# Kernel optimization log

Measured on AMD Instinct MI355X. Metric: run time of the kernel, lower is better.

Reference implementation:

```python
import jax, jax.numpy as jnp
import numpy as np
import math

EMBED = 512
KDIM = 512
VDIM = 512
H = 8
HD = EMBED // H
N = 2048
L = 2048
B = 4


def setup_inputs() -> dict:
    key = jax.random.key(0)
    ks = jax.random.split(key, 14)
    s = 1.0 / math.sqrt(EMBED)
    return {
        "q": jax.random.normal(ks[0], (N, B, EMBED), jnp.float32),
        "k": jax.random.normal(ks[1], (L, B, KDIM), jnp.float32),
        "v": jax.random.normal(ks[2], (L, B, VDIM), jnp.float32),
        "pe1": jax.random.normal(ks[3], (B, N, 3), jnp.float32),
        "pe2": jax.random.normal(ks[4], (L, 3), jnp.float32),
        "Wq": jax.random.normal(ks[5], (EMBED, EMBED), jnp.float32) * s,
        "bq": jnp.zeros((EMBED,), jnp.float32),
        "Wk": jax.random.normal(ks[6], (EMBED, KDIM), jnp.float32) * s,
        "bk": jnp.zeros((EMBED,), jnp.float32),
        "Wv": jax.random.normal(ks[7], (EMBED, VDIM), jnp.float32) * s,
        "bv": jnp.zeros((EMBED,), jnp.float32),
        "Wo": jax.random.normal(ks[8], (EMBED, EMBED), jnp.float32) * s,
        "bo": jnp.zeros((EMBED,), jnp.float32),
    }


def reference(q, k, v, pe1, pe2, Wq, bq, Wk, bk, Wv, bv, Wo, bo):
    n, b, _ = q.shape
    l = k.shape[0]
    # projections (nn.Linear: x @ W.T + b)
    qp = q @ Wq.T + bq  # (n, b, E)
    kp = k @ Wk.T + bk  # (l, b, E)
    vp = v @ Wv.T + bv  # (l, b, E)
    # split heads -> (b, H, n, hd)
    qh = qp.reshape(n, b, H, HD).transpose(1, 2, 0, 3)
    kh = kp.reshape(l, b, H, HD).transpose(1, 2, 0, 3)
    vh = vp.reshape(l, b, H, HD).transpose(1, 2, 0, 3)
    # relative PE bias: (b, n, l), broadcast over heads
    pe_scores = jnp.einsum('bnc,lc->bnl', pe1, pe2)[:, None, :, :]
    scores = (jnp.einsum('bhnd,bhld->bhnl', qh, kh) + pe_scores) / math.sqrt(HD)
    attn = jax.nn.softmax(scores, axis=-1)
    out = jnp.einsum('bhnl,bhld->bhnd', attn, vh)  # (b, H, n, hd)
    out = out.transpose(2, 0, 1, 3).reshape(n, b, EMBED)
    return out @ Wo.T + bo
```

## Files before the change

kernel.cpp:

```cpp
#include <hip/hip_runtime.h>
#include <math.h>

#define EMBED 512
#define HDIM 64
#define NHEADS 8
#define SEQ_N 2048
#define SEQ_L 2048
#define BATCH 4
#define MROWS (SEQ_N*BATCH)
#define BE (BATCH*EMBED)

#define QSCALE 0.18033688f

typedef _Float16 f16;
typedef _Float16 half8 __attribute__((ext_vector_type(8)));
typedef _Float16 half4 __attribute__((ext_vector_type(4)));
typedef _Float16 half2v __attribute__((ext_vector_type(2)));
typedef float floatx4 __attribute__((ext_vector_type(4)));
typedef float floatx16 __attribute__((ext_vector_type(16)));

static __device__ inline float fast_exp2(float x) {
#if __has_builtin(__builtin_amdgcn_exp2f)
  return __builtin_amdgcn_exp2f(x);
#else
  return __expf(x * 0.69314718056f);
#endif
}

static __device__ inline half2v pk2(float a, float b) {
#if __has_builtin(__builtin_amdgcn_cvt_pkrtz)
  return __builtin_bit_cast(half2v, __builtin_amdgcn_cvt_pkrtz(a, b));
#else
  half2v o; o[0] = (f16)a; o[1] = (f16)b; return o;
#endif
}

static __device__ inline void gload16(const void* g, void* l) {
  __builtin_amdgcn_global_load_lds(
      (__attribute__((address_space(1))) void*)(g),
      (__attribute__((address_space(3))) void*)(l), 16, 0, 0);
}

__global__ __launch_bounds__(256) void cvt_all(const float* __restrict__ q,
                                               const float* __restrict__ k,
                                               const float* __restrict__ v,
                                               const float* __restrict__ Wq,
                                               const float* __restrict__ Wk,
                                               const float* __restrict__ Wv,
                                               const float* __restrict__ Wo,
                                               f16* __restrict__ qb, f16* __restrict__ kb,
                                               f16* __restrict__ vb, f16* __restrict__ Wb) {
  const long TOK = (long)MROWS * EMBED;
  const long WSZ = (long)EMBED * EMBED;
  int y = blockIdx.y;
  long i = ((long)blockIdx.x * 256 + threadIdx.x) * 4;
  if (y < 3) {
    if (i < TOK) {
      const float* s = y == 0 ? q : y == 1 ? k : v;
      f16* d = y == 0 ? qb : y == 1 ? kb : vb;
      float4 f = *reinterpret_cast<const float4*>(s + i);
      half4 o; o[0] = (f16)f.x; o[1] = (f16)f.y; o[2] = (f16)f.z; o[3] = (f16)f.w;
      *reinterpret_cast<half4*>(d + i) = o;
    }
  } else {
    if (i < 4 * WSZ) {
      int sel = (int)(i >> 18);
      long off = i & (WSZ - 1);
      const float* s = sel == 0 ? Wq : sel == 1 ? Wk : sel == 2 ? Wv : Wo;
      float4 f = *reinterpret_cast<const float4*>(s + off);
      half4 o; o[0] = (f16)f.x; o[1] = (f16)f.y; o[2] = (f16)f.z; o[3] = (f16)f.w;
      *reinterpret_cast<half4*>(Wb + i) = o;
    }
  }
}

__global__ __launch_bounds__(256) void gemm_qkv(const f16* __restrict__ A0,
                                                const f16* __restrict__ A1,
                                                const f16* __restrict__ A2,
                                                const f16* __restrict__ W0,
                                                const f16* __restrict__ W1,
                                                const f16* __restrict__ W2,
                                                const float* __restrict__ b0,
                                                const float* __restrict__ b1,
                                                const float* __restrict__ b2,
                                                f16* __restrict__ C0, f16* __restrict__ C1,
                                                f16* __restrict__ C2t) {
  __shared__ alignas(16) f16 As[128 * 32];
  __shared__ alignas(16) f16 Bs[128 * 32];
  const int sel = blockIdx.y >> 2;
  const f16* A = sel == 0 ? A0 : sel == 1 ? A1 : A2;
  const f16* Bt = sel == 0 ? W0 : sel == 1 ? W1 : W2;
  const float* bias = sel == 0 ? b0 : sel == 1 ? b1 : b2;
  const float scl = sel == 0 ? QSCALE : 1.0f;
  const int tid = threadIdx.x;
  const int wave = tid >> 6, lane = tid & 63, quad = lane >> 4, l16 = lane & 15;
  const int wm = wave & 1, wn = wave >> 1;
  const long m0 = (long)blockIdx.x * 128;
  const long n0 = (long)(blockIdx.y & 3) * 128;
  floatx4 acc[4][4] = {};
  const int srow = lane >> 2;
  const int scol = (lane & 3) * 8;

  for (int k0 = 0; k0 < EMBED; k0 += 32) {
    __syncthreads();
    gload16(A + (m0 + wave * 32 + srow) * EMBED + k0 + scol, &As[(wave * 32) * 32]);
    gload16(A + (m0 + wave * 32 + 16 + srow) * EMBED + k0 + scol, &As[(wave * 32 + 16) * 32]);
    gload16(Bt + (n0 + wave * 32 + srow) * EMBED + k0 + scol, &Bs[(wave * 32) * 32]);
    gload16(Bt + (n0 + wave * 32 + 16 + srow) * EMBED + k0 + scol, &Bs[(wave * 32 + 16) * 32]);
    __syncthreads();
    half8 af[4], bf[4];
#pragma unroll
    for (int i = 0; i < 4; ++i)
      af[i] = *reinterpret_cast<const half8*>(&As[(wm * 64 + i * 16 + l16) * 32 + quad * 8]);
#pragma unroll
    for (int j = 0; j < 4; ++j)
      bf[j] = *reinterpret_cast<const half8*>(&Bs[(wn * 64 + j * 16 + l16) * 32 + quad * 8]);
#pragma unroll
    for (int i = 0; i < 4; ++i)
#pragma unroll
      for (int j = 0; j < 4; ++j)
        acc[i][j] = __builtin_amdgcn_mfma_f32_16x16x32_f16(af[i], bf[j], acc[i][j], 0, 0, 0);
  }
#pragma unroll
  for (int i = 0; i < 4; ++i)
#pragma unroll
    for (int r = 0; r < 4; ++r) {
      long row = m0 + wm * 64 + i * 16 + quad * 4 + r;
#pragma unroll
      for (int j = 0; j < 4; ++j) {
        long col = n0 + wn * 64 + j * 16 + l16;
        float val = (acc[i][j][r] + bias[col]) * scl;
        if (sel == 2) {
          long bq = row & 3, ltok = row >> 2;
          long hh = col >> 6, dd = col & 63;
          C2t[(((bq << 3) + hh) * 64 + dd) * 2048 + ltok] = (f16)val;
        } else {
          f16* C = sel == 0 ? C0 : C1;
          C[row * EMBED + col] = (f16)val;
        }
      }
    }
}

__global__ __launch_bounds__(256) void gemm_out(const f16* __restrict__ A,
                                                const f16* __restrict__ Bt,
                                                const float* __restrict__ bias,
                                                float* __restrict__ C) {
  __shared__ alignas(16) f16 As[128 * 32];
  __shared__ alignas(16) f16 Bs[64 * 32];
  const int tid = threadIdx.x;
  const int wave = tid >> 6, lane = tid & 63, quad = lane >> 4, l16 = lane & 15;
  const long m0 = (long)blockIdx.x * 128;
  const long n0 = (long)blockIdx.y * 64;
  floatx4 acc[2][4] = {};
  const int srow = lane >> 2;
  const int scol = (lane & 3) * 8;

  for (int k0 = 0; k0 < EMBED; k0 += 32) {
    __syncthreads();
    gload16(A + (m0 + wave * 32 + srow) * EMBED + k0 + scol, &As[(wave * 32) * 32]);
    gload16(A + (m0 + wave * 32 + 16 + srow) * EMBED + k0 + scol, &As[(wave * 32 + 16) * 32]);
    gload16(Bt + (n0 + wave * 16 + srow) * EMBED + k0 + scol, &Bs[(wave * 16) * 32]);
    __syncthreads();
    half8 af[2], bf[4];
#pragma unroll
    for (int i = 0; i < 2; ++i)
      af[i] = *reinterpret_cast<const half8*>(&As[(wave * 32 + i * 16 + l16) * 32 + quad * 8]);
#pragma unroll
    for (int j = 0; j < 4; ++j)
      bf[j] = *reinterpret_cast<const half8*>(&Bs[(j * 16 + l16) * 32 + quad * 8]);
#pragma unroll
    for (int i = 0; i < 2; ++i)
#pragma unroll
      for (int j = 0; j < 4; ++j)
        acc[i][j] = __builtin_amdgcn_mfma_f32_16x16x32_f16(af[i], bf[j], acc[i][j], 0, 0, 0);
  }
#pragma unroll
  for (int i = 0; i < 2; ++i)
#pragma unroll
    for (int r = 0; r < 4; ++r) {
      long row = m0 + wave * 32 + i * 16 + quad * 4 + r;
#pragma unroll
      for (int j = 0; j < 4; ++j) {
        long col = n0 + j * 16 + l16;
        C[row * EMBED + col] = acc[i][j][r] + bias[col];
      }
    }
}

#define KST 88
#define VST 136
#define NCHUNK (SEQ_L / 128)
#define LDSB (128 * KST * 2 + 64 * VST * 2)
__global__ __launch_bounds__(512, 4) void attn_flash(const f16* __restrict__ qp,
                                                     const f16* __restrict__ kp,
                                                     const f16* __restrict__ vt,
                                                     const float* __restrict__ pe1,
                                                     const float* __restrict__ pe2,
                                                     f16* __restrict__ ao) {
  __shared__ alignas(16) unsigned char smem[LDSB];
  f16* Ks = reinterpret_cast<f16*>(smem);
  f16* Vt = reinterpret_cast<f16*>(smem + 128 * KST * 2);
  float* comb = reinterpret_cast<float*>(smem);
  const int tid = threadIdx.x, wave = tid >> 6, lane = tid & 63;
  const int m = lane & 31, h = lane >> 5;
  const int strip = wave & 3, half = wave >> 2;
  const int n0 = blockIdx.x * 128;
  const int b = blockIdx.y >> 3, hd = blockIdx.y & 7;
  const long headoff = (long)b * EMBED + hd * HDIM;
  const long vhead = (long)blockIdx.y * 64 * 2048;

  for (int c = tid; c < 1024; c += 512) {
    int r = c >> 3, col = (c & 7) * 8;
    *reinterpret_cast<uint4*>(&Ks[r * KST + col]) =
        *reinterpret_cast<const uint4*>(qp + (long)(n0 + r) * BE + headoff + col);
    int rv = c >> 4, cv = (c & 15) * 8;
    *reinterpret_cast<uint4*>(&Vt[rv * VST + cv]) =
        *reinterpret_cast<const uint4*>(vt + vhead + (long)rv * 2048 + 0 + cv);
  }
  {
    const uint4 z4 = {0, 0, 0, 0};
    const uint2 z2 = {0, 0};
    int r = tid >> 2, s = tid & 3;
    if (s == 0) *reinterpret_cast<uint2*>(&Ks[r * KST + 68]) = z2;
    else if (s == 1) *reinterpret_cast<uint4*>(&Ks[r * KST + 72]) = z4;
    else if (s == 2) *reinterpret_cast<uint4*>(&Ks[r * KST + 80]) = z4;
  }
  if (tid < 128) {
    long base = ((long)b * SEQ_N + n0 + tid) * 3;
    half4 v8;
    v8[0] = (f16)(pe1[base + 0] * QSCALE);
    v8[1] = (f16)(pe1[base + 1] * QSCALE);
    v8[2] = (f16)(pe1[base + 2] * QSCALE);
    v8[3] = (f16)0.f;
    *reinterpret_cast<half4*>(&Ks[tid * KST + 64]) = v8;
  }
  __syncthreads();

  half8 qf[5];
#pragma unroll
  for (int e = 0; e < 5; ++e)
    qf[e] = *reinterpret_cast<const half8*>(&Ks[(strip * 32 + m) * KST + e * 16 + h * 8]);
  __syncthreads();

  for (int c = tid; c < 1024; c += 512) {
    int r = c >> 3, col = (c & 7) * 8;
    *reinterpret_cast<uint4*>(&Ks[r * KST + col]) =
        *reinterpret_cast<const uint4*>(kp + (long)(0 + r) * BE + headoff + col);
  }
  if (tid < 128) {
    long bb = (long)(0 + tid) * 3;
    half4 p2;
    p2[0] = (f16)pe2[bb + 0]; p2[1] = (f16)pe2[bb + 1];
    p2[2] = (f16)pe2[bb + 2]; p2[3] = (f16)0.f;
    *reinterpret_cast<half4*>(&Ks[tid * KST + 64]) = p2;
  }

  floatx16 oacc[2] = {};
  float lpart = 0.f;

#pragma unroll 1
  for (int c = 0; c < NCHUNK; ++c) {
    __syncthreads();
#pragma unroll
    for (int tt = 0; tt < 2; ++tt) {
      const int t = half * 2 + tt;
      floatx16 st = {};
#pragma unroll
      for (int e = 0; e < 5; ++e) {
        half8 kf = *reinterpret_cast<const half8*>(&Ks[(t * 32 + m) * KST + e * 16 + h * 8]);
        st = __builtin_amdgcn_mfma_f32_32x32x16_f16(kf, qf[e], st, 0, 0, 0);
      }
      float p[16];
#pragma unroll
      for (int r = 0; r < 16; ++r) {
        p[r] = fast_exp2(st[r]);
        lpart += p[r];
      }
#pragma unroll
      for (int s = 0; s < 4; ++s) {
        half2v u0 = pk2(p[4 * s + 0], p[4 * s + 1]);
        half2v u1 = pk2(p[4 * s + 2], p[4 * s + 3]);
        half4 bp;
        bp[0] = u0[0]; bp[1] = u0[1]; bp[2] = u1[0]; bp[3] = u1[1];
        int lcol = t * 32 + s * 8 + h * 4;
#pragma unroll
        for (int dt = 0; dt < 2; ++dt) {
          half4 vf = *reinterpret_cast<const half4*>(&Vt[(dt * 32 + m) * VST + lcol]);
          oacc[dt] = __builtin_amdgcn_mfma_f32_32x32x8f16(vf, bp, oacc[dt], 0, 0, 0);
        }
      }
    }
    __syncthreads();
    if (c + 1 < NCHUNK) {
      const int l0 = (c + 1) * 128;
      for (int cc = tid; cc < 1024; cc += 512) {
        int r = cc >> 3, col = (cc & 7) * 8;
        *reinterpret_cast<uint4*>(&Ks[r * KST + col]) =
            *reinterpret_cast<const uint4*>(kp + (long)(l0 + r) * BE + headoff + col);
        int rv = cc >> 4, cv = (cc & 15) * 8;
        *reinterpret_cast<uint4*>(&Vt[rv * VST + cv]) =
            *reinterpret_cast<const uint4*>(vt + vhead + (long)rv * 2048 + l0 + cv);
      }
      if (tid < 128) {
        long bb = (long)(l0 + tid) * 3;
        half4 p2;
        p2[0] = (f16)pe2[bb + 0]; p2[1] = (f16)pe2[bb + 1];
        p2[2] = (f16)pe2[bb + 2]; p2[3] = (f16)0.f;
        *reinterpret_cast<half4*>(&Ks[tid * KST + 64]) = p2;
      }
    }
  }

  lpart += __shfl_xor(lpart, 32);

  if (half == 1) {
    float* dst = comb + (strip * 64 + lane) * 33;
#pragma unroll
    for (int dt = 0; dt < 2; ++dt)
#pragma unroll
      for (int x = 0; x < 16; ++x) dst[dt * 16 + x] = oacc[dt][x];
    dst[32] = lpart;
  }
  __syncthreads();
  if (half == 0) {
    const float* src = comb + (strip * 64 + lane) * 33;
#pragma unroll
    for (int dt = 0; dt < 2; ++dt)
#pragma unroll
      for (int x = 0; x < 16; ++x) oacc[dt][x] += src[dt * 16 + x];
    float inv = 1.f / (lpart + src[32]);
    long qrow = n0 + strip * 32 + m;
#pragma unroll
    for (int dt = 0; dt < 2; ++dt)
#pragma unroll
      for (int g = 0; g < 4; ++g) {
        half4 o4;
#pragma unroll
        for (int x = 0; x < 4; ++x) o4[x] = (f16)(oacc[dt][4 * g + x] * inv);
        int d = dt * 32 + 8 * g + 4 * h;
        *reinterpret_cast<half4*>(ao + qrow * BE + headoff + d) = o4;
      }
  }
}

extern "C" void kernel_launch(void* const* d_in, const int* in_sizes, int n_in,
                              void* d_out, int out_size, void* d_ws, size_t ws_size,
                              hipStream_t stream) {
  const float* q   = (const float*)d_in[0];
  const float* k   = (const float*)d_in[1];
  const float* v   = (const float*)d_in[2];
  const float* pe1 = (const float*)d_in[3];
  const float* pe2 = (const float*)d_in[4];
  const float* Wq  = (const float*)d_in[5];
  const float* bq  = (const float*)d_in[6];
  const float* Wk  = (const float*)d_in[7];
  const float* bk  = (const float*)d_in[8];
  const float* Wv  = (const float*)d_in[9];
  const float* bv  = (const float*)d_in[10];
  const float* Wo  = (const float*)d_in[11];
  const float* bo  = (const float*)d_in[12];
  float* out = (float*)d_out;

  f16* ws = (f16*)d_ws;
  const long TOK = (long)MROWS * EMBED;
  const long WSZ = (long)EMBED * EMBED;
  f16* qb  = ws;
  f16* kb  = qb + TOK;
  f16* vb  = kb + TOK;
  f16* Wqb = vb + TOK;
  f16* Wkb = Wqb + WSZ;
  f16* Wvb = Wkb + WSZ;
  f16* Wob = Wvb + WSZ;
  f16* qpb = Wob + WSZ;
  f16* kpb = qpb + TOK;
  f16* vtb = kpb + TOK;
  f16* aob = vtb + TOK;

  cvt_all<<<dim3(4096, 4), 256, 0, stream>>>(q, k, v, Wq, Wk, Wv, Wo, qb, kb, vb, Wqb);

  gemm_qkv<<<dim3(MROWS / 128, 12), 256, 0, stream>>>(qb, kb, vb, Wqb, Wkb, Wvb,
                                                      bq, bk, bv, qpb, kpb, vtb);

  attn_flash<<<dim3(SEQ_N / 128, BATCH * NHEADS), 512, 0, stream>>>(qpb, kpb, vtb, pe1, pe2, aob);

  gemm_out<<<dim3(MROWS / 128, EMBED / 64), 256, 0, stream>>>(aob, Wob, bo, out);
}
```

Before: 203.4 us.

## Double-buffer GEMM LDS tiles and prefetch attention K/V chunks into registers

Both projection GEMMs now use two LDS buffers, so the global-to-LDS loads for the next K-slice are issued before the MFMAs on the current slice, leaving one barrier per step instead of two. The attention kernel issues global loads for the next K/V/pe2 chunk into registers at the top of each chunk, ahead of the compute, and writes them to LDS after the barrier. This hides global memory latency behind math at the cost of doubled LDS in the GEMMs and extra VGPRs in attention, which may reduce occupancy.

```diff
diff --git a/kernel.cpp b/kernel.cpp
--- a/kernel.cpp
+++ b/kernel.cpp
@@ -85,8 +85,8 @@
                                                 const float* __restrict__ b2,
                                                 f16* __restrict__ C0, f16* __restrict__ C1,
                                                 f16* __restrict__ C2t) {
-  __shared__ alignas(16) f16 As[128 * 32];
-  __shared__ alignas(16) f16 Bs[128 * 32];
+  __shared__ alignas(16) f16 As[2][128 * 32];
+  __shared__ alignas(16) f16 Bs[2][128 * 32];
   const int sel = blockIdx.y >> 2;
   const f16* A = sel == 0 ? A0 : sel == 1 ? A1 : A2;
   const f16* Bt = sel == 0 ? W0 : sel == 1 ? W1 : W2;
@@ -97,29 +97,48 @@
   const int wm = wave & 1, wn = wave >> 1;
   const long m0 = (long)blockIdx.x * 128;
   const long n0 = (long)(blockIdx.y & 3) * 128;
-  floatx4 acc[4][4] = {};
   const int srow = lane >> 2;
   const int scol = (lane & 3) * 8;
 
-  for (int k0 = 0; k0 < EMBED; k0 += 32) {
-    __syncthreads();
-    gload16(A + (m0 + wave * 32 + srow) * EMBED + k0 + scol, &As[(wave * 32) * 32]);
-    gload16(A + (m0 + wave * 32 + 16 + srow) * EMBED + k0 + scol, &As[(wave * 32 + 16) * 32]);
-    gload16(Bt + (n0 + wave * 32 + srow) * EMBED + k0 + scol, &Bs[(wave * 32) * 32]);
-    gload16(Bt + (n0 + wave * 32 + 16 + srow) * EMBED + k0 + scol, &Bs[(wave * 32 + 16) * 32]);
-    __syncthreads();
+  const f16* Ag0 = A + (m0 + wave * 32 + srow) * EMBED + scol;
+  const f16* Ag1 = A + (m0 + wave * 32 + 16 + srow) * EMBED + scol;
+  const f16* Bg0 = Bt + (n0 + wave * 32 + srow) * EMBED + scol;
+  const f16* Bg1 = Bt + (n0 + wave * 32 + 16 + srow) * EMBED + scol;
+
+  gload16(Ag0, &As[0][(wave * 32) * 32]);
+  gload16(Ag1, &As[0][(wave * 32 + 16) * 32]);
+  gload16(Bg0, &Bs[0][(wave * 32) * 32]);
+  gload16(Bg1, &Bs[0][(wave * 32 + 16) * 32]);
+  floatx4 acc[4][4] = {};
+  asm volatile("s_waitcnt vmcnt(0)" ::: "memory");
+  __builtin_amdgcn_s_barrier();
+
+#pragma unroll
+  for (int ks = 0; ks < 16; ++ks) {
+    const int cur = ks & 1;
+    if (ks + 1 < 16) {
+      const int k1 = (ks + 1) * 32;
+      gload16(Ag0 + k1, &As[cur ^ 1][(wave * 32) * 32]);
+      gload16(Ag1 + k1, &As[cur ^ 1][(wave * 32 + 16) * 32]);
+      gload16(Bg0 + k1, &Bs[cur ^ 1][(wave * 32) * 32]);
+      gload16(Bg1 + k1, &Bs[cur ^ 1][(wave * 32 + 16) * 32]);
+    }
     half8 af[4], bf[4];
 #pragma unroll
     for (int i = 0; i < 4; ++i)
-      af[i] = *reinterpret_cast<const half8*>(&As[(wm * 64 + i * 16 + l16) * 32 + quad * 8]);
+      af[i] = *reinterpret_cast<const half8*>(&As[cur][(wm * 64 + i * 16 + l16) * 32 + quad * 8]);
 #pragma unroll
     for (int j = 0; j < 4; ++j)
-      bf[j] = *reinterpret_cast<const half8*>(&Bs[(wn * 64 + j * 16 + l16) * 32 + quad * 8]);
+      bf[j] = *reinterpret_cast<const half8*>(&Bs[cur][(wn * 64 + j * 16 + l16) * 32 + quad * 8]);
 #pragma unroll
     for (int i = 0; i < 4; ++i)
 #pragma unroll
       for (int j = 0; j < 4; ++j)
         acc[i][j] = __builtin_amdgcn_mfma_f32_16x16x32_f16(af[i], bf[j], acc[i][j], 0, 0, 0);
+    if (ks + 1 < 16) {
+      asm volatile("s_waitcnt vmcnt(0)" ::: "memory");
+      __builtin_amdgcn_s_barrier();
+    }
   }
 #pragma unroll
   for (int i = 0; i < 4; ++i)
@@ -146,34 +165,51 @@
                                                 const f16* __restrict__ Bt,
                                                 const float* __restrict__ bias,
                                                 float* __restrict__ C) {
-  __shared__ alignas(16) f16 As[128 * 32];
-  __shared__ alignas(16) f16 Bs[64 * 32];
+  __shared__ alignas(16) f16 As[2][128 * 32];
+  __shared__ alignas(16) f16 Bs[2][64 * 32];
   const int tid = threadIdx.x;
   const int wave = tid >> 6, lane = tid & 63, quad = lane >> 4, l16 = lane & 15;
   const long m0 = (long)blockIdx.x * 128;
   const long n0 = (long)blockIdx.y * 64;
-  floatx4 acc[2][4] = {};
   const int srow = lane >> 2;
   const int scol = (lane & 3) * 8;
 
-  for (int k0 = 0; k0 < EMBED; k0 += 32) {
-    __syncthreads();
-    gload16(A + (m0 + wave * 32 + srow) * EMBED + k0 + scol, &As[(wave * 32) * 32]);
-    gload16(A + (m0 + wave * 32 + 16 + srow) * EMBED + k0 + scol, &As[(wave * 32 + 16) * 32]);
-    gload16(Bt + (n0 + wave * 16 + srow) * EMBED + k0 + scol, &Bs[(wave * 16) * 32]);
-    __syncthreads();
+  const f16* Ag0 = A + (m0 + wave * 32 + srow) * EMBED + scol;
+  const f16* Ag1 = A + (m0 + wave * 32 + 16 + srow) * EMBED + scol;
+  const f16* Bg0 = Bt + (n0 + wave * 16 + srow) * EMBED + scol;
+
+  gload16(Ag0, &As[0][(wave * 32) * 32]);
+  gload16(Ag1, &As[0][(wave * 32 + 16) * 32]);
+  gload16(Bg0, &Bs[0][(wave * 16) * 32]);
+  floatx4 acc[2][4] = {};
+  asm volatile("s_waitcnt vmcnt(0)" ::: "memory");
+  __builtin_amdgcn_s_barrier();
+
+#pragma unroll
+  for (int ks = 0; ks < 16; ++ks) {
+    const int cur = ks & 1;
+    if (ks + 1 < 16) {
+      const int k1 = (ks + 1) * 32;
+      gload16(Ag0 + k1, &As[cur ^ 1][(wave * 32) * 32]);
+      gload16(Ag1 + k1, &As[cur ^ 1][(wave * 32 + 16) * 32]);
+      gload16(Bg0 + k1, &Bs[cur ^ 1][(wave * 16) * 32]);
+    }
     half8 af[2], bf[4];
 #pragma unroll
     for (int i = 0; i < 2; ++i)
-      af[i] = *reinterpret_cast<const half8*>(&As[(wave * 32 + i * 16 + l16) * 32 + quad * 8]);
+      af[i] = *reinterpret_cast<const half8*>(&As[cur][(wave * 32 + i * 16 + l16) * 32 + quad * 8]);
 #pragma unroll
     for (int j = 0; j < 4; ++j)
-      bf[j] = *reinterpret_cast<const half8*>(&Bs[(j * 16 + l16) * 32 + quad * 8]);
+      bf[j] = *reinterpret_cast<const half8*>(&Bs[cur][(j * 16 + l16) * 32 + quad * 8]);
 #pragma unroll
     for (int i = 0; i < 2; ++i)
 #pragma unroll
       for (int j = 0; j < 4; ++j)
         acc[i][j] = __builtin_amdgcn_mfma_f32_16x16x32_f16(af[i], bf[j], acc[i][j], 0, 0, 0);
+    if (ks + 1 < 16) {
+      asm volatile("s_waitcnt vmcnt(0)" ::: "memory");
+      __builtin_amdgcn_s_barrier();
+    }
   }
 #pragma unroll
   for (int i = 0; i < 2; ++i)
@@ -262,6 +298,32 @@
 #pragma unroll 1
   for (int c = 0; c < NCHUNK; ++c) {
     __syncthreads();
+
+    uint4 kreg0, kreg1, vreg0, vreg1;
+    float p2x, p2y, p2z;
+    const bool pf = (c + 1 < NCHUNK);
+    if (pf) {
+      const int l0 = (c + 1) * 128;
+      {
+        int r = tid >> 3, col = (tid & 7) * 8;
+        kreg0 = *reinterpret_cast<const uint4*>(kp + (long)(l0 + r) * BE + headoff + col);
+        int rv = tid >> 4, cv = (tid & 15) * 8;
+        vreg0 = *reinterpret_cast<const uint4*>(vt + vhead + (long)rv * 2048 + l0 + cv);
+      }
+      {
+        int c2 = tid + 512;
+        int r = c2 >> 3, col = (c2 & 7) * 8;
+        kreg1 = *reinterpret_cast<const uint4*>(kp + (long)(l0 + r) * BE + headoff + col);
+        int rv = c2 >> 4, cv = (c2 & 15) * 8;
+        vreg1 = *reinterpret_cast<const uint4*>(vt + vhead + (long)rv * 2048 + l0 + cv);
+      }
+      if (tid < 128) {
+        long bb = (long)(l0 + tid) * 3;
+        p2x = pe2[bb + 0]; p2y = pe2[bb + 1]; p2z = pe2[bb + 2];
+      }
+      __builtin_amdgcn_sched_barrier(0);
+    }
+
 #pragma unroll
     for (int tt = 0; tt < 2; ++tt) {
       const int t = half * 2 + tt;
@@ -292,21 +354,24 @@
       }
     }
     __syncthreads();
-    if (c + 1 < NCHUNK) {
-      const int l0 = (c + 1) * 128;
-      for (int cc = tid; cc < 1024; cc += 512) {
-        int r = cc >> 3, col = (cc & 7) * 8;
-        *reinterpret_cast<uint4*>(&Ks[r * KST + col]) =
-            *reinterpret_cast<const uint4*>(kp + (long)(l0 + r) * BE + headoff + col);
-        int rv = cc >> 4, cv = (cc & 15) * 8;
-        *reinterpret_cast<uint4*>(&Vt[rv * VST + cv]) =
-            *reinterpret_cast<const uint4*>(vt + vhead + (long)rv * 2048 + l0 + cv);
+
+    if (pf) {
+      {
+        int r = tid >> 3, col = (tid & 7) * 8;
+        *reinterpret_cast<uint4*>(&Ks[r * KST + col]) = kreg0;
+        int rv = tid >> 4, cv = (tid & 15) * 8;
+        *reinterpret_cast<uint4*>(&Vt[rv * VST + cv]) = vreg0;
+      }
+      {
+        int c2 = tid + 512;
+        int r = c2 >> 3, col = (c2 & 7) * 8;
+        *reinterpret_cast<uint4*>(&Ks[r * KST + col]) = kreg1;
+        int rv = c2 >> 4, cv = (c2 & 15) * 8;
+        *reinterpret_cast<uint4*>(&Vt[rv * VST + cv]) = vreg1;
       }
       if (tid < 128) {
-        long bb = (long)(l0 + tid) * 3;
         half4 p2;
-        p2[0] = (f16)pe2[bb + 0]; p2[1] = (f16)pe2[bb + 1];
-        p2[2] = (f16)pe2[bb + 2]; p2[3] = (f16)0.f;
+        p2[0] = (f16)p2x; p2[1] = (f16)p2y; p2[2] = (f16)p2z; p2[3] = (f16)0.f;
         *reinterpret_cast<half4*>(&Ks[tid * KST + 64]) = p2;
       }
     }
```

Result: slower. 215.5 us (+5.9%).
